# Optimization experiments

Hardware: AMD Instinct MI355X
Metric: run time of the kernel (lower is better)

Reference implementation:

```python
import jax, jax.numpy as jnp
import numpy as np


def setup_inputs() -> dict:
    key = jax.random.key(0)
    k1, k2 = jax.random.split(key)
    x = jax.random.normal(k1, (16, 8192, 128), dtype=jnp.float32)
    embed = jax.random.normal(k2, (1024, 128), dtype=jnp.float32)
    return {"x": x, "embed": embed}


def reference(x, embed):
    # preprocess: flatten leading dims -> (N, d)
    shape = x.shape
    xf = x.reshape(-1, shape[-1])  # (N, d)
    # quantize: negative squared Euclidean distance, argmax over codebook
    dist = (2.0 * (xf @ embed.T)
            - jnp.sum(xf * xf, axis=1, keepdims=True)
            - jnp.sum(embed * embed, axis=1)[None, :])
    embed_ind = jnp.argmax(dist, axis=-1)  # (N,)
    # postprocess indices back to input leading shape
    embed_ind = embed_ind.reshape(shape[:-1])
    # dequantize: embedding lookup
    quantize = embed[embed_ind]  # (..., d)
    return embed_ind, quantize
```

## Files before the change

### kernel.cpp

```cpp
#include <hip/hip_runtime.h>
#include <math.h>


typedef __attribute__((ext_vector_type(8)))  short short8_t;
typedef __attribute__((ext_vector_type(16))) float floatx16;

constexpr int D        = 128;
constexpr int KCODES   = 1024;
constexpr int NTILES   = 32;
constexpr int ROWS_BLK = 128;
constexpr float TAU    = 0.015f;

constexpr size_t WS_COUNTER = 0;
constexpr size_t WS_CSQ     = 256;
constexpr size_t WS_EHI     = 8192;
constexpr size_t WS_ELO     = WS_EHI + 262144;
constexpr size_t WS_LIST    = WS_ELO + 262144;

#define GLOBAL_AS __attribute__((address_space(1)))
#define LDS_AS    __attribute__((address_space(3)))

__device__ inline unsigned short bf16_rne(float v, float* back) {
    unsigned u = __float_as_uint(v);
    unsigned r = (u + 0x7FFFu + ((u >> 16) & 1u)) >> 16;
    *back = __uint_as_float(r << 16);
    return (unsigned short)r;
}

__global__ void ecb_prep(const float* __restrict__ embed, float* __restrict__ csq,
                         unsigned short* __restrict__ ehi, unsigned short* __restrict__ elo,
                         unsigned int* __restrict__ counter) {
    int n = blockIdx.x * 64 + threadIdx.x;
    if (n == 0) *counter = 0u;
    if (n >= KCODES) return;
    const int t = n >> 5, nn = n & 31, nm = nn & 15;
    const float* row = embed + (size_t)n * D;
    const size_t tb = (size_t)t * 32 * D + (size_t)nn * D;
    float s = 0.f;
#pragma unroll
    for (int cc = 0; cc < 16; ++cc) {
        float4 a  = *(const float4*)(row + cc * 8);
        float4 bq = *(const float4*)(row + cc * 8 + 4);
        s = fmaf(a.x, a.x, s);  s = fmaf(a.y, a.y, s);
        s = fmaf(a.z, a.z, s);  s = fmaf(a.w, a.w, s);
        s = fmaf(bq.x, bq.x, s); s = fmaf(bq.y, bq.y, s);
        s = fmaf(bq.z, bq.z, s); s = fmaf(bq.w, bq.w, s);
        float vv[8] = {a.x, a.y, a.z, a.w, bq.x, bq.y, bq.z, bq.w};
        unsigned short h[8], l[8];
#pragma unroll
        for (int j = 0; j < 8; ++j) {
            float hb, db;
            h[j] = bf16_rne(vv[j], &hb);
            l[j] = bf16_rne(vv[j] - hb, &db);
        }
        uint4 ph, pl;
        ph.x = (unsigned)h[0] | ((unsigned)h[1] << 16);
        ph.y = (unsigned)h[2] | ((unsigned)h[3] << 16);
        ph.z = (unsigned)h[4] | ((unsigned)h[5] << 16);
        ph.w = (unsigned)h[6] | ((unsigned)h[7] << 16);
        pl.x = (unsigned)l[0] | ((unsigned)l[1] << 16);
        pl.y = (unsigned)l[2] | ((unsigned)l[3] << 16);
        pl.z = (unsigned)l[4] | ((unsigned)l[5] << 16);
        pl.w = (unsigned)l[6] | ((unsigned)l[7] << 16);
        size_t dst = tb + (size_t)((cc ^ nm) * 8);
        *(uint4*)(ehi + dst) = ph;
        *(uint4*)(elo + dst) = pl;
    }
    csq[n] = s;
}

__global__ __launch_bounds__(256, 2)
void ecb_main(const float* __restrict__ x,
              const unsigned short* __restrict__ ehi, const unsigned short* __restrict__ elo,
              const float* __restrict__ csq, const float* __restrict__ embed,
              float* __restrict__ out_idx, float* __restrict__ out_q,
              unsigned int* __restrict__ counter, unsigned int* __restrict__ list) {
    __shared__ unsigned short ebuf[2][2][4096];
    __shared__ float scsq[KCODES];
    __shared__ int   sidx[ROWS_BLK];

    const int tid  = threadIdx.x;
    const int lane = tid & 63, wave = tid >> 6;
    const int col  = lane & 31, h = lane >> 5, colm = col & 15;
    const long rowblk = (long)blockIdx.x * ROWS_BLK;
    const int  roww   = wave * 32;

    for (int i = tid; i < KCODES; i += 256) scsq[i] = csq[i];

    short8_t ah[8], al[8];
    {
        const float* xr = x + (rowblk + roww + col) * (long)D + h * 8;
#pragma unroll
        for (int c = 0; c < 8; ++c) {
            float4 a  = *(const float4*)(xr + c * 16);
            float4 bq = *(const float4*)(xr + c * 16 + 4);
            float vv[8] = {a.x, a.y, a.z, a.w, bq.x, bq.y, bq.z, bq.w};
            short8_t fh, fl;
#pragma unroll
            for (int j = 0; j < 8; ++j) {
                float hb, db;
                fh[j] = (short)bf16_rne(vv[j], &hb);
                fl[j] = (short)bf16_rne(vv[j] - hb, &db);
            }
            ah[c] = fh;
            al[c] = fl;
        }
    }

    auto stage = [&](int t, int b) {
        const char* gh = (const char*)(ehi) + (size_t)t * 8192;
        const char* gl = (const char*)(elo) + (size_t)t * 8192;
        char* lh = (char*)&ebuf[b][0][0];
        char* ll = (char*)&ebuf[b][1][0];
#pragma unroll
        for (int i = 0; i < 2; ++i) {
            int off = i * 4096 + wave * 1024;
            __builtin_amdgcn_global_load_lds((const GLOBAL_AS unsigned int*)(gh + off + lane * 16),
                                             (LDS_AS unsigned int*)(lh + off), 16, 0, 0);
            __builtin_amdgcn_global_load_lds((const GLOBAL_AS unsigned int*)(gl + off + lane * 16),
                                             (LDS_AS unsigned int*)(ll + off), 16, 0, 0);
        }
    };

    float v1[16], v2[16];
#pragma unroll
    for (int j = 0; j < 16; ++j) { v1[j] = -INFINITY; v2[j] = -INFINITY; }

    stage(0, 0);
    __syncthreads();

#pragma unroll 1
    for (int t = 0; t < NTILES; ++t) {
        const int b = t & 1;
        if (t + 1 < NTILES) stage(t + 1, (t + 1) & 1);

        floatx16 acc;
#pragma unroll
        for (int i = 0; i < 16; ++i) acc[i] = 0.f;

#pragma unroll
        for (int s = 0; s < 8; ++s) {
            const int cc = 2 * s + h;
            const int idx = (col * 16 + (cc ^ colm)) * 8;
            short8_t bh = *(const short8_t*)&ebuf[b][0][idx];
            short8_t bl = *(const short8_t*)&ebuf[b][1][idx];
            acc = __builtin_amdgcn_mfma_f32_32x32x16_bf16(ah[s], bh, acc, 0, 0, 0);
            acc = __builtin_amdgcn_mfma_f32_32x32x16_bf16(al[s], bh, acc, 0, 0, 0);
            acc = __builtin_amdgcn_mfma_f32_32x32x16_bf16(ah[s], bl, acc, 0, 0, 0);
        }

        const float cs = scsq[t * 32 + col];
#pragma unroll
        for (int j = 0; j < 16; ++j) {
            float sc = fmaf(2.f, acc[j], -cs);
            unsigned u = (__float_as_uint(sc) & ~31u) | (unsigned)t;
            float cand = __uint_as_float(u);
            float mn = fminf(v1[j], cand);
            v1[j] = fmaxf(v1[j], cand);
            v2[j] = fmaxf(v2[j], mn);
        }
        __syncthreads();
    }

#pragma unroll
    for (int j = 0; j < 16; ++j) {
        float a1 = v1[j], a2 = v2[j];
        int   c1 = ((__float_as_uint(a1) & 31u) << 5) | col;
#pragma unroll
        for (int m = 1; m < 32; m <<= 1) {
            float o1 = __shfl_xor(a1, m, 64);
            int   oc = __shfl_xor(c1, m, 64);
            float o2 = __shfl_xor(a2, m, 64);
            float lo = fminf(a1, o1);
            if (o1 > a1) { a1 = o1; c1 = oc; }
            a2 = fmaxf(fmaxf(a2, o2), lo);
        }
        if (col == j) {
            int row_local = roww + (j & 3) + 8 * (j >> 2) + 4 * h;
            long grow = rowblk + row_local;
            sidx[row_local] = c1;
            out_idx[grow] = (float)c1;
            if (a1 - a2 < TAU) {
                unsigned p = atomicAdd(counter, 1u);
                list[p] = (unsigned)grow;
            }
        }
    }
    __syncthreads();

    for (int i = tid; i < ROWS_BLK * 32; i += 256) {
        int r = i >> 5, q = i & 31;
        int code = sidx[r];
        float4 v = *(const float4*)(embed + (size_t)code * D + q * 4);
        *(float4*)(out_q + (rowblk + r) * (long)D + q * 4) = v;
    }
}

__global__ __launch_bounds__(256)
void ecb_recheck(const float* __restrict__ x, const float* __restrict__ embed,
                 const float* __restrict__ csq,
                 float* __restrict__ out_idx, float* __restrict__ out_q,
                 const unsigned int* __restrict__ counter,
                 const unsigned int* __restrict__ list, int N) {
    __shared__ float xs[D];
    __shared__ float bv[256];
    __shared__ int   bi[256];
    const int tid = threadIdx.x;
    unsigned cnt = *counter;
    if (cnt > (unsigned)N) cnt = (unsigned)N;

    for (unsigned it = blockIdx.x; it < cnt; it += gridDim.x) {
        const long row = (long)list[it];
        if (tid < 32) *(float4*)&xs[tid * 4] = *(const float4*)(x + row * D + tid * 4);
        __syncthreads();

        float best = -INFINITY; int bidx = 0;
#pragma unroll
        for (int g = 0; g < 4; ++g) {
            int code = tid + g * 256;
            const float* er = embed + (size_t)code * D;
            float dot = 0.f;
#pragma unroll
            for (int k = 0; k < 32; ++k) {
                float4 e = *(const float4*)(er + k * 4);
                dot = fmaf(xs[k * 4 + 0], e.x, dot);
                dot = fmaf(xs[k * 4 + 1], e.y, dot);
                dot = fmaf(xs[k * 4 + 2], e.z, dot);
                dot = fmaf(xs[k * 4 + 3], e.w, dot);
            }
            float sc = fmaf(2.f, dot, -csq[code]);
            if (sc > best || (sc == best && code < bidx)) { best = sc; bidx = code; }
        }
        bv[tid] = best; bi[tid] = bidx;
        __syncthreads();
        for (int s = 128; s > 0; s >>= 1) {
            if (tid < s) {
                float ov = bv[tid + s]; int oi = bi[tid + s];
                if (ov > bv[tid] || (ov == bv[tid] && oi < bi[tid])) { bv[tid] = ov; bi[tid] = oi; }
            }
            __syncthreads();
        }
        const int win = bi[0];
        if (tid == 0) out_idx[row] = (float)win;
        if (tid < 32) {
            float4 v = *(const float4*)(embed + (size_t)win * D + tid * 4);
            *(float4*)(out_q + row * D + tid * 4) = v;
        }
        __syncthreads();
    }
}

extern "C" void kernel_launch(void* const* d_in, const int* in_sizes, int n_in,
                              void* d_out, int out_size, void* d_ws, size_t ws_size,
                              hipStream_t stream) {
    const float* x     = (const float*)d_in[0];
    const float* embed = (const float*)d_in[1];
    const int N = in_sizes[0] / D;
    char* ws = (char*)d_ws;
    unsigned int*   counter = (unsigned int*)(ws + WS_COUNTER);
    float*          csq     = (float*)(ws + WS_CSQ);
    unsigned short* ehi     = (unsigned short*)(ws + WS_EHI);
    unsigned short* elo     = (unsigned short*)(ws + WS_ELO);
    unsigned int*   list    = (unsigned int*)(ws + WS_LIST);
    float* out_idx = (float*)d_out;
    float* out_q   = out_idx + N;

    hipLaunchKernelGGL(ecb_prep, dim3(16), dim3(64), 0, stream, embed, csq, ehi, elo, counter);
    hipLaunchKernelGGL(ecb_main, dim3(N / ROWS_BLK), dim3(256), 0, stream,
                       x, ehi, elo, csq, embed, out_idx, out_q, counter, list);
    hipLaunchKernelGGL(ecb_recheck, dim3(512), dim3(256), 0, stream,
                       x, embed, csq, out_idx, out_q, counter, list, N);
}
```

Measured before the change: 249.8 us.

## Split MFMA accumulators, drop LDS csq copy, transpose embed for recheck

The main kernel now uses two independent MFMA accumulator chains so back-to-back MFMAs are less serially dependent. It reads the code norms straight from global memory instead of staging them in shared memory, and raises the launch-bounds occupancy hint from 2 to 3 blocks. The recheck kernel reads a transposed copy of the codebook, built in the prep kernel, so that each thread's reads across the block are coalesced float4 loads; its grid grows to 1024 blocks and the candidate list is capped. The extra accumulator and the occupancy hint may increase register pressure or cause spills, and the prep kernel now does strided transposed writes.

```diff
diff --git a/kernel.cpp b/kernel.cpp
--- a/kernel.cpp
+++ b/kernel.cpp
@@ -10,12 +10,14 @@
 constexpr int NTILES   = 32;
 constexpr int ROWS_BLK = 128;
 constexpr float TAU    = 0.015f;
+constexpr unsigned LIST_CAP = 65536;
 
 constexpr size_t WS_COUNTER = 0;
 constexpr size_t WS_CSQ     = 256;
 constexpr size_t WS_EHI     = 8192;
 constexpr size_t WS_ELO     = WS_EHI + 262144;
 constexpr size_t WS_LIST    = WS_ELO + 262144;
+constexpr size_t WS_EMBT    = WS_LIST + 262144;
 
 #define GLOBAL_AS __attribute__((address_space(1)))
 #define LDS_AS    __attribute__((address_space(3)))
@@ -29,7 +31,7 @@
 
 __global__ void ecb_prep(const float* __restrict__ embed, float* __restrict__ csq,
                          unsigned short* __restrict__ ehi, unsigned short* __restrict__ elo,
-                         unsigned int* __restrict__ counter) {
+                         float* __restrict__ embT, unsigned int* __restrict__ counter) {
     int n = blockIdx.x * 64 + threadIdx.x;
     if (n == 0) *counter = 0u;
     if (n >= KCODES) return;
@@ -46,6 +48,8 @@
         s = fmaf(bq.x, bq.x, s); s = fmaf(bq.y, bq.y, s);
         s = fmaf(bq.z, bq.z, s); s = fmaf(bq.w, bq.w, s);
         float vv[8] = {a.x, a.y, a.z, a.w, bq.x, bq.y, bq.z, bq.w};
+#pragma unroll
+        for (int j = 0; j < 8; ++j) embT[(size_t)(cc * 8 + j) * KCODES + n] = vv[j];
         unsigned short h[8], l[8];
 #pragma unroll
         for (int j = 0; j < 8; ++j) {
@@ -69,23 +73,20 @@
     csq[n] = s;
 }
 
-__global__ __launch_bounds__(256, 2)
+__global__ __launch_bounds__(256, 3)
 void ecb_main(const float* __restrict__ x,
               const unsigned short* __restrict__ ehi, const unsigned short* __restrict__ elo,
               const float* __restrict__ csq, const float* __restrict__ embed,
               float* __restrict__ out_idx, float* __restrict__ out_q,
               unsigned int* __restrict__ counter, unsigned int* __restrict__ list) {
     __shared__ unsigned short ebuf[2][2][4096];
-    __shared__ float scsq[KCODES];
-    __shared__ int   sidx[ROWS_BLK];
+    __shared__ int sidx[ROWS_BLK];
 
     const int tid  = threadIdx.x;
     const int lane = tid & 63, wave = tid >> 6;
     const int col  = lane & 31, h = lane >> 5, colm = col & 15;
     const long rowblk = (long)blockIdx.x * ROWS_BLK;
     const int  roww   = wave * 32;
-
-    for (int i = tid; i < KCODES; i += 256) scsq[i] = csq[i];
 
     short8_t ah[8], al[8];
     {
@@ -134,9 +135,11 @@
         const int b = t & 1;
         if (t + 1 < NTILES) stage(t + 1, (t + 1) & 1);
 
-        floatx16 acc;
-#pragma unroll
-        for (int i = 0; i < 16; ++i) acc[i] = 0.f;
+        const float cs = csq[t * 32 + col];
+
+        floatx16 accA, accB;
+#pragma unroll
+        for (int i = 0; i < 16; ++i) { accA[i] = 0.f; accB[i] = 0.f; }
 
 #pragma unroll
         for (int s = 0; s < 8; ++s) {
@@ -144,15 +147,14 @@
             const int idx = (col * 16 + (cc ^ colm)) * 8;
             short8_t bh = *(const short8_t*)&ebuf[b][0][idx];
             short8_t bl = *(const short8_t*)&ebuf[b][1][idx];
-            acc = __builtin_amdgcn_mfma_f32_32x32x16_bf16(ah[s], bh, acc, 0, 0, 0);
-            acc = __builtin_amdgcn_mfma_f32_32x32x16_bf16(al[s], bh, acc, 0, 0, 0);
-            acc = __builtin_amdgcn_mfma_f32_32x32x16_bf16(ah[s], bl, acc, 0, 0, 0);
-        }
-
-        const float cs = scsq[t * 32 + col];
+            accA = __builtin_amdgcn_mfma_f32_32x32x16_bf16(ah[s], bh, accA, 0, 0, 0);
+            accB = __builtin_amdgcn_mfma_f32_32x32x16_bf16(al[s], bh, accB, 0, 0, 0);
+            accB = __builtin_amdgcn_mfma_f32_32x32x16_bf16(ah[s], bl, accB, 0, 0, 0);
+        }
+
 #pragma unroll
         for (int j = 0; j < 16; ++j) {
-            float sc = fmaf(2.f, acc[j], -cs);
+            float sc = fmaf(2.f, accA[j] + accB[j], -cs);
             unsigned u = (__float_as_uint(sc) & ~31u) | (unsigned)t;
             float cand = __uint_as_float(u);
             float mn = fminf(v1[j], cand);
@@ -182,7 +184,7 @@
             out_idx[grow] = (float)c1;
             if (a1 - a2 < TAU) {
                 unsigned p = atomicAdd(counter, 1u);
-                list[p] = (unsigned)grow;
+                if (p < LIST_CAP) list[p] = (unsigned)grow;
             }
         }
     }
@@ -197,40 +199,42 @@
 }
 
 __global__ __launch_bounds__(256)
-void ecb_recheck(const float* __restrict__ x, const float* __restrict__ embed,
-                 const float* __restrict__ csq,
+void ecb_recheck(const float* __restrict__ x, const float* __restrict__ embT,
+                 const float* __restrict__ embed, const float* __restrict__ csq,
                  float* __restrict__ out_idx, float* __restrict__ out_q,
                  const unsigned int* __restrict__ counter,
-                 const unsigned int* __restrict__ list, int N) {
+                 const unsigned int* __restrict__ list) {
     __shared__ float xs[D];
     __shared__ float bv[256];
     __shared__ int   bi[256];
     const int tid = threadIdx.x;
     unsigned cnt = *counter;
-    if (cnt > (unsigned)N) cnt = (unsigned)N;
+    if (cnt > LIST_CAP) cnt = LIST_CAP;
+    const float4* eT = (const float4*)embT;
 
     for (unsigned it = blockIdx.x; it < cnt; it += gridDim.x) {
         const long row = (long)list[it];
         if (tid < 32) *(float4*)&xs[tid * 4] = *(const float4*)(x + row * D + tid * 4);
         __syncthreads();
 
+        float4 dot = {0.f, 0.f, 0.f, 0.f};
+        for (int k = 0; k < D; ++k) {
+            float xv = xs[k];
+            float4 e = eT[(size_t)k * 256 + tid];
+            dot.x = fmaf(xv, e.x, dot.x);
+            dot.y = fmaf(xv, e.y, dot.y);
+            dot.z = fmaf(xv, e.z, dot.z);
+            dot.w = fmaf(xv, e.w, dot.w);
+        }
+        const int c0 = tid * 4;
         float best = -INFINITY; int bidx = 0;
-#pragma unroll
-        for (int g = 0; g < 4; ++g) {
-            int code = tid + g * 256;
-            const float* er = embed + (size_t)code * D;
-            float dot = 0.f;
-#pragma unroll
-            for (int k = 0; k < 32; ++k) {
-                float4 e = *(const float4*)(er + k * 4);
-                dot = fmaf(xs[k * 4 + 0], e.x, dot);
-                dot = fmaf(xs[k * 4 + 1], e.y, dot);
-                dot = fmaf(xs[k * 4 + 2], e.z, dot);
-                dot = fmaf(xs[k * 4 + 3], e.w, dot);
-            }
-            float sc = fmaf(2.f, dot, -csq[code]);
-            if (sc > best || (sc == best && code < bidx)) { best = sc; bidx = code; }
-        }
+        float scs[4] = {fmaf(2.f, dot.x, -csq[c0]),
+                        fmaf(2.f, dot.y, -csq[c0 + 1]),
+                        fmaf(2.f, dot.z, -csq[c0 + 2]),
+                        fmaf(2.f, dot.w, -csq[c0 + 3])};
+#pragma unroll
+        for (int i = 0; i < 4; ++i)
+            if (scs[i] > best) { best = scs[i]; bidx = c0 + i; }
         bv[tid] = best; bi[tid] = bidx;
         __syncthreads();
         for (int s = 128; s > 0; s >>= 1) {
@@ -262,12 +266,14 @@
     unsigned short* ehi     = (unsigned short*)(ws + WS_EHI);
     unsigned short* elo     = (unsigned short*)(ws + WS_ELO);
     unsigned int*   list    = (unsigned int*)(ws + WS_LIST);
+    float*          embT    = (float*)(ws + WS_EMBT);
     float* out_idx = (float*)d_out;
     float* out_q   = out_idx + N;
 
-    hipLaunchKernelGGL(ecb_prep, dim3(16), dim3(64), 0, stream, embed, csq, ehi, elo, counter);
+    hipLaunchKernelGGL(ecb_prep, dim3(16), dim3(64), 0, stream,
+                       embed, csq, ehi, elo, embT, counter);
     hipLaunchKernelGGL(ecb_main, dim3(N / ROWS_BLK), dim3(256), 0, stream,
                        x, ehi, elo, csq, embed, out_idx, out_q, counter, list);
-    hipLaunchKernelGGL(ecb_recheck, dim3(512), dim3(256), 0, stream,
-                       x, embed, csq, out_idx, out_q, counter, list, N);
-}
+    hipLaunchKernelGGL(ecb_recheck, dim3(1024), dim3(256), 0, stream,
+                       x, embT, embed, csq, out_idx, out_q, counter, list);
+}
```

New measurement: 231.4 us. 7.4% less time.
